# Kernel optimization log

Measured on AMD Instinct MI355X. Metric: run time of the kernel, lower is better.

The kernel has to match this reference:

```python
import jax, jax.numpy as jnp
import numpy as np

IOU_THRESHOLD = 0.5
ROIS_NUMBER = 256


def setup_inputs() -> dict:
    key = jax.random.key(0)
    k1, k2, k3 = jax.random.split(key, 3)
    B, N = 8, 4096
    scores = jax.random.uniform(k1, (B, N, 1), dtype=jnp.float32)
    xy = jax.random.uniform(k2, (B, N, 2), dtype=jnp.float32) * 100.0
    wh = jax.random.uniform(k3, (B, N, 2), dtype=jnp.float32) * 20.0 + 1.0
    return {"input": jnp.concatenate([scores, xy, wh], axis=-1)}


def _make_corners(regs):
    # regs: [N,4] = (x, y, w, h); TF uses floor-div by 2 (`//`) on floats
    x, y, w, h = regs[:, 0], regs[:, 1], regs[:, 2], regs[:, 3]
    ws = w // 2
    hs = h // 2
    return jnp.stack([x - ws, y - hs, x + ws, y + hs], axis=-1)


def _nms_single(preds, key):
    # preds: [N,5] = (score, x, y, w, h)
    N = preds.shape[0]
    scores = preds[:, 0]
    boxes = _make_corners(preds[:, 1:])
    order = jnp.argsort(-scores)                       # descending score
    b = boxes[order]
    x1, y1, x2, y2 = b[:, 0], b[:, 1], b[:, 2], b[:, 3]
    area = (x2 - x1) * (y2 - y1)
    # pairwise IoU [N,N] (selection only -> stop_gradient)
    ix1 = jnp.maximum(x1[:, None], x1[None, :])
    iy1 = jnp.maximum(y1[:, None], y1[None, :])
    ix2 = jnp.minimum(x2[:, None], x2[None, :])
    iy2 = jnp.minimum(y2[:, None], y2[None, :])
    inter = jnp.maximum(ix2 - ix1, 0.0) * jnp.maximum(iy2 - iy1, 0.0)
    union = area[:, None] + area[None, :] - inter
    iou = jax.lax.stop_gradient(jnp.where(union > 0, inter / union, 0.0))

    idx = jnp.arange(N)

    def step(suppressed, i):
        keep_i = ~suppressed[i]
        suppressed = suppressed | (keep_i & (iou[i] > IOU_THRESHOLD) & (idx > i))
        return suppressed, keep_i

    _, keep = jax.lax.scan(step, jnp.zeros((N,), bool), idx)

    # first ROIS_NUMBER kept positions (in score order); N marks "not kept"
    pos = jnp.sort(jnp.where(keep, idx, N))[:ROIS_NUMBER]
    valid = pos < N
    sel = order[jnp.minimum(pos, N - 1)]
    rand_idx = jax.random.randint(key, (ROIS_NUMBER,), 0, N)
    sel = jnp.where(valid, sel, rand_idx)              # pad with random regions
    return preds[sel][:, 1:]                           # [ROIS,4] = (x,y,w,h)


def reference(input) -> jnp.ndarray:
    B = input.shape[0]
    keys = jax.random.split(jax.random.key(42), B)
    return jax.vmap(_nms_single)(input, keys)
```

## Files before the change

### kernel.cpp

```cpp
#include <hip/hip_runtime.h>
#include <stdint.h>

#pragma clang fp contract(off)

#define NMS_B 8
#define NMS_N 4096
#define ROIS 256

typedef unsigned long long u64;
typedef unsigned int u32;

__device__ __forceinline__ int lds_slot(int e) { return e + (e >> 2); }

__device__ __forceinline__ bool sup_pred(float4 rc, float rh, float4 cc, float ch) {
    float iw = fmaxf(fminf(rc.z, cc.z) - fmaxf(rc.x, cc.x), 0.0f);
    float ih = fmaxf(fminf(rc.w, cc.w) - fmaxf(rc.y, cc.y), 0.0f);
    float inter = iw * ih;
    return inter > fmaf(-0.5f, inter, rh + ch);
}

__global__ __launch_bounds__(1024, 1) void nms_all(
        const float* __restrict__ in, u32* __restrict__ sortedIdx,
        float4* __restrict__ crn, float* __restrict__ ha,
        float* __restrict__ outp) {
    __shared__ u64 sm[5120];
    __shared__ int kept[ROIS];
    __shared__ int s_selCount, s_B, s_needFull;
    const int b = blockIdx.x, t = threadIdx.x;
    const int lane = t & 63, wid = t >> 6;
    const size_t base = (size_t)b * NMS_N;

    u32* hist = (u32*)sm;
    u32* pp   = (u32*)sm + 4096;
    u32* qq   = (u32*)sm + 5120;
    float sc[4];
    int   bk[4];
    #pragma unroll
    for (int r = 0; r < 4; ++r) {
        int e = t + 1024 * r;
        sc[r] = in[(base + e) * 5];
        int bb = (int)(sc[r] * 4096.0f);
        bk[r] = bb > 4095 ? 4095 : bb;
    }
    for (int i = t; i < 4096; i += 1024) hist[i] = 0;
    if (t == 0) { s_selCount = 0; s_needFull = 0; }
    __syncthreads();
    #pragma unroll
    for (int r = 0; r < 4; ++r) atomicAdd(&hist[bk[r]], 1u);
    __syncthreads();
    pp[t] = hist[4 * t] + hist[4 * t + 1] + hist[4 * t + 2] + hist[4 * t + 3];
    __syncthreads();
    if (t < 64) {
        u32 s = 0;
        for (int i = 0; i < 16; ++i) s += pp[16 * t + i];
        qq[t] = s;
    }
    __syncthreads();
    if (t == 0) {
        int acc = 0, L = 0;
        for (int l = 63; l >= 0; --l) { acc += (int)qq[l]; if (acc >= 512) { L = l; break; } }
        int rem = 512 - (acc - (int)qq[L]);
        int acc2 = 0, T = 16 * L;
        for (int i = 16 * L + 15; i >= 16 * L; --i) { acc2 += (int)pp[i]; if (acc2 >= rem) { T = i; break; } }
        int rem2 = rem - (acc2 - (int)pp[T]);
        int acc3 = 0, B = 4 * T;
        for (int bb = 4 * T + 3; bb >= 4 * T; --bb) { acc3 += (int)hist[bb]; if (acc3 >= rem2) { B = bb; break; } }
        s_B = B;
    }
    __syncthreads();

    u64* selKey = sm + 2560;
    const int B = s_B;
    #pragma unroll
    for (int r = 0; r < 4; ++r) {
        if (bk[r] >= B) {
            int slot = atomicAdd(&s_selCount, 1);
            if (slot < 1024) {
                int e = t + 1024 * r;
                selKey[slot] = ((u64)(~__float_as_uint(sc[r])) << 32) | (u32)e;
            }
        }
    }
    __syncthreads();
    const int selCount = s_selCount;
    const bool fullPath = (selCount > 1024);

    if (!fullPath) {
        u64 kk = (t < selCount) ? selKey[t] : ~0ULL;
        for (int k = 2; k <= 1024; k <<= 1) {
            int j = k >> 1;
            for (; j >= 64; j >>= 1) {
                sm[lds_slot(t)] = kk;
                __syncthreads();
                u64 part = sm[lds_slot(t ^ j)];
                bool up = ((t & k) == 0), lower = ((t & j) == 0);
                u64 mn = kk < part ? kk : part, mx = kk < part ? part : kk;
                kk = (up == lower) ? mn : mx;
                __syncthreads();
            }
            for (; j >= 1; j >>= 1) {
                u64 part = __shfl_xor(kk, j, 64);
                bool up = ((t & k) == 0), lower = ((t & j) == 0);
                u64 mn = kk < part ? kk : part, mx = kk < part ? part : kk;
                kk = (up == lower) ? mn : mx;
            }
        }
        selKey[t] = kk;
        __syncthreads();

        float4* crn_s = (float4*)((char*)sm + 28672);
        float*  ha_s  = (float*)((char*)sm + 36864);
        u32*    sidx_s = (u32*)((char*)sm + 38912);
        if (t < 512) {
            u32 orig = (u32)selKey[t];
            const float* bp = in + (base + orig) * 5;
            float x = bp[1], y = bp[2], w = bp[3], h = bp[4];
            float ws_ = floorf(w * 0.5f), hs_ = floorf(h * 0.5f);
            float4 c4 = make_float4(x - ws_, y - hs_, x + ws_, y + hs_);
            crn_s[t] = c4;
            ha_s[t] = 0.5f * ((c4.z - c4.x) * (c4.w - c4.y));
            sidx_s[t] = orig;
        }
        for (int r = t; r < ROIS; r += 1024) kept[r] = 0;
        __syncthreads();

        u64* h_lds = sm;
        for (int u = wid; u < 36; u += 16) {
            int kr = 0;
            while ((kr + 1) * (kr + 2) / 2 <= u) ++kr;
            int w = u - kr * (kr + 1) / 2;
            float4 myc = crn_s[64 * kr + lane];
            float  myh = ha_s[64 * kr + lane];
            u64 word = 0;
            #pragma unroll 4
            for (int q = 0; q < 64; ++q) {
                bool p = sup_pred(crn_s[64 * w + q], ha_s[64 * w + q], myc, myh);
                word |= ((u64)(p ? 1u : 0u)) << q;
            }
            h_lds[u * 64 + lane] = word;
        }
        __syncthreads();

        if (t < 64) {
            int count = 0;
            u32 f[8];
            #pragma unroll
            for (int k = 0; k < 8; ++k) f[k] = 1u;
            bool done = false;
            #pragma unroll
            for (int g = 0; g < 8; ++g) {
                if (!done) {
                    u64 hgg = h_lds[(g * (g + 1) / 2 + g) * 64 + lane];
                    u64 kb = 0;
                    u64 avail = __ballot(f[g] != 0);
                    while (avail != 0 && count < ROIS) {
                        int r = __builtin_ctzll(avail);
                        if (lane == 0) kept[count] = g * 64 + r;
                        ++count;
                        kb |= 1ULL << r;
                        u32 bit = (u32)(hgg >> r) & 1u;
                        f[g] &= (bit ^ 1u) & (u32)(lane != r);
                        avail = __ballot(f[g] != 0);
                    }
                    if (count >= ROIS) {
                        done = true;
                    } else {
                        #pragma unroll
                        for (int k2 = g + 1; k2 < 8; ++k2)
                            f[k2] &= (u32)((h_lds[(k2 * (k2 + 1) / 2 + g) * 64 + lane] & kb) == 0);
                    }
                }
            }
            if (t == 0) s_needFull = (count >= ROIS) ? 0 : 1;
        }
        __syncthreads();
    }

    if (fullPath || s_needFull) {
        u64 key[4];
        #pragma unroll
        for (int r = 0; r < 4; ++r) {
            int e = 4 * t + r;
            float s = in[(base + e) * 5];
            key[r] = ((u64)(~__float_as_uint(s)) << 32) | (u32)e;
        }
        for (int k = 2; k <= 4096; k <<= 1) {
            int j = k >> 1;
            if (j >= 256) {
                #pragma unroll
                for (int r = 0; r < 4; ++r) sm[lds_slot(4 * t + r)] = key[r];
                __syncthreads();
                for (; j >= 256; j >>= 1) {
                    for (int el = t; el < 4096; el += 1024) {
                        int p = el ^ j;
                        if (p > el) {
                            u64 a = sm[lds_slot(el)], cc = sm[lds_slot(p)];
                            bool up = ((el & k) == 0);
                            if ((a > cc) == up) { sm[lds_slot(el)] = cc; sm[lds_slot(p)] = a; }
                        }
                    }
                    __syncthreads();
                }
                #pragma unroll
                for (int r = 0; r < 4; ++r) key[r] = sm[lds_slot(4 * t + r)];
            }
            for (; j >= 4; j >>= 1) {
                int d = j >> 2;
                #pragma unroll
                for (int r = 0; r < 4; ++r) {
                    int e = 4 * t + r;
                    u64 mine = key[r];
                    u64 part = __shfl_xor(mine, d, 64);
                    bool up = ((e & k) == 0);
                    bool lower = ((e & j) == 0);
                    u64 mn = (mine < part) ? mine : part;
                    u64 mx = (mine < part) ? part : mine;
                    key[r] = (up == lower) ? mn : mx;
                }
            }
            for (; j >= 1; j >>= 1) {
                #pragma unroll
                for (int r = 0; r < 4; ++r) {
                    int pr = r | j;
                    if (((r & j) == 0) && pr < 4) {
                        int e = 4 * t + r;
                        bool up = ((e & k) == 0);
                        u64 a = key[r], cc = key[pr];
                        if ((a > cc) == up) { key[r] = cc; key[pr] = a; }
                    }
                }
            }
        }
        __syncthreads();

        u64*    h2 = sm;
        float4* crn2 = (float4*)(sm + 2304);
        float*  ha2  = (float*)(sm + 2304 + 1024);

        #pragma unroll
        for (int r = 0; r < 4; ++r) {
            int e = 4 * t + r;
            u32 orig = (u32)key[r];
            const float* bp = in + (base + orig) * 5;
            float x = bp[1], y = bp[2], w = bp[3], h = bp[4];
            float ws_ = floorf(w * 0.5f), hs_ = floorf(h * 0.5f);
            float4 c4 = make_float4(x - ws_, y - hs_, x + ws_, y + hs_);
            float hv = 0.5f * ((c4.z - c4.x) * (c4.w - c4.y));
            size_t g = base + e;
            sortedIdx[g] = orig;
            crn[g] = c4;
            ha[g] = hv;
            if (e < 512) { crn2[e] = c4; ha2[e] = hv; }
        }
        for (int r = t; r < ROIS; r += 1024) kept[r] = 0;
        __syncthreads();

        for (int u = wid; u < 36; u += 16) {
            int kr = 0;
            while ((kr + 1) * (kr + 2) / 2 <= u) ++kr;
            int w = u - kr * (kr + 1) / 2;
            float4 myc = crn2[64 * kr + lane];
            float  myh = ha2[64 * kr + lane];
            u64 word = 0;
            #pragma unroll 4
            for (int q = 0; q < 64; ++q) {
                bool p = sup_pred(crn2[64 * w + q], ha2[64 * w + q], myc, myh);
                word |= ((u64)(p ? 1u : 0u)) << q;
            }
            h2[(size_t)u * 64 + lane] = word;
        }
        __syncthreads();

        if (t < 64) {
            int count = 0;
            u32 f[8];
            #pragma unroll
            for (int k = 0; k < 8; ++k) f[k] = 1u;
            bool done = false;
            #pragma unroll
            for (int g = 0; g < 8; ++g) {
                if (!done) {
                    u64 hgg = h2[(size_t)(g * (g + 1) / 2 + g) * 64 + lane];
                    u64 kb = 0;
                    u64 avail = __ballot(f[g] != 0);
                    while (avail != 0 && count < ROIS) {
                        int r = __builtin_ctzll(avail);
                        if (lane == 0) kept[count] = g * 64 + r;
                        ++count;
                        kb |= 1ULL << r;
                        u32 bit = (u32)(hgg >> r) & 1u;
                        f[g] &= (bit ^ 1u) & (u32)(lane != r);
                        avail = __ballot(f[g] != 0);
                    }
                    if (count >= ROIS) {
                        done = true;
                    } else {
                        #pragma unroll
                        for (int k2 = g + 1; k2 < 8; ++k2)
                            f[k2] &= (u32)((h2[(size_t)(k2 * (k2 + 1) / 2 + g) * 64 + lane] & kb) == 0);
                    }
                }
            }
            if (count < ROIS) {
                for (int Wp = 4; Wp < 32 && count < ROIS; ++Wp) {
                    const int cLo = 128 * Wp + lane, cHi = cLo + 64;
                    float4 cL = crn[base + cLo]; float hL = ha[base + cLo];
                    float4 cH = crn[base + cHi]; float hH = ha[base + cHi];
                    u32 fLo = 1u, fHi = 1u;
                    for (int j2 = 0; j2 < count; ++j2) {
                        int pos = kept[j2];
                        float4 kc = crn[base + pos]; float kh = ha[base + pos];
                        fLo &= (u32)(!sup_pred(kc, kh, cL, hL));
                        fHi &= (u32)(!sup_pred(kc, kh, cH, hH));
                    }
                    u64 curLo0 = 0, curHi0 = 0, curHi1 = 0;
                    for (int r = 0; r < 64; ++r) {
                        float4 rc = crn[base + 128 * Wp + r]; float rh = ha[base + 128 * Wp + r];
                        curLo0 |= ((u64)(sup_pred(rc, rh, cL, hL) ? 1u : 0u)) << r;
                        curHi0 |= ((u64)(sup_pred(rc, rh, cH, hH) ? 1u : 0u)) << r;
                    }
                    for (int r = 0; r < 64; ++r) {
                        float4 rc = crn[base + 128 * Wp + 64 + r]; float rh = ha[base + 128 * Wp + 64 + r];
                        curHi1 |= ((u64)(sup_pred(rc, rh, cH, hH) ? 1u : 0u)) << r;
                    }
                    u64 availLo = __ballot(fLo != 0);
                    while (availLo != 0 && count < ROIS) {
                        int r = __builtin_ctzll(availLo);
                        if (lane == 0) kept[count] = Wp * 128 + r;
                        ++count;
                        fLo &= (u32)(((curLo0 >> r) & 1ULL) ^ 1ULL) & (u32)(lane != r);
                        fHi &= (u32)(((curHi0 >> r) & 1ULL) ^ 1ULL);
                        availLo = __ballot(fLo != 0);
                    }
                    u64 availHi = __ballot(fHi != 0);
                    while (availHi != 0 && count < ROIS) {
                        int r = __builtin_ctzll(availHi);
                        if (lane == 0) kept[count] = Wp * 128 + 64 + r;
                        ++count;
                        fHi &= (u32)(((curHi1 >> r) & 1ULL) ^ 1ULL) & (u32)(lane != r);
                        availHi = __ballot(fHi != 0);
                    }
                }
            }
        }
    }
    __syncthreads();

    const bool usedFull = fullPath || (s_needFull != 0);
    if (t < ROIS) {
        int pos = kept[t];
        int orig = usedFull ? (int)sortedIdx[base + pos]
                            : (int)((u32*)((char*)sm + 38912))[pos];
        const float* bp = in + (base + orig) * 5;
        ((float4*)outp)[(size_t)b * ROIS + t] =
            make_float4(bp[1], bp[2], bp[3], bp[4]);
    }
}

extern "C" void kernel_launch(void* const* d_in, const int* in_sizes, int n_in,
                              void* d_out, int out_size, void* d_ws, size_t ws_size,
                              hipStream_t stream) {
    const float* in = (const float*)d_in[0];
    float* out = (float*)d_out;
    char* ws = (char*)d_ws;

    u32* sortedIdx = (u32*)ws;                 size_t off = (size_t)NMS_B * NMS_N * 4;
    float4* crn = (float4*)(ws + off);         off += (size_t)NMS_B * NMS_N * 16;
    float* ha = (float*)(ws + off);            off += (size_t)NMS_B * NMS_N * 4;

    nms_all<<<NMS_B, 1024, 0, stream>>>(in, sortedIdx, crn, ha, out);
}
```

Baseline: 103.1 us.

## Sort four keys per thread, aggregate selection atomics, split IoU mask words

The 1024-element bitonic sort now runs on 256 threads holding four keys each. Only the strides of 256 and up go through LDS with barriers; smaller strides use wave shuffles and in-register compare-swaps, which removes most block-wide syncs. Candidate selection uses one ballot-based atomic per wave instead of one atomic per element. The IoU mask computation is split into 32-bit half-words so twice as many wave tasks share the work. Shared memory is re-laid out with dedicated regions, which raises LDS use, and a clamp of negative bucket indices is added.

```diff
diff --git a/kernel.cpp b/kernel.cpp
--- a/kernel.cpp
+++ b/kernel.cpp
@@ -23,16 +23,23 @@
         const float* __restrict__ in, u32* __restrict__ sortedIdx,
         float4* __restrict__ crn, float* __restrict__ ha,
         float* __restrict__ outp) {
-    __shared__ u64 sm[5120];
+    __shared__ u64 sm[8736];
     __shared__ int kept[ROIS];
     __shared__ int s_selCount, s_B, s_needFull;
     const int b = blockIdx.x, t = threadIdx.x;
     const int lane = t & 63, wid = t >> 6;
     const size_t base = (size_t)b * NMS_N;
 
-    u32* hist = (u32*)sm;
-    u32* pp   = (u32*)sm + 4096;
-    u32* qq   = (u32*)sm + 5120;
+    u32*    hist   = (u32*)sm;
+    u32*    pp     = (u32*)(sm + 2048);
+    u32*    qq     = (u32*)(sm + 2560);
+    u64*    selKey = sm + 2592;
+    u64*    sortA  = sm + 3616;
+    float4* crn_s  = (float4*)(sm + 4896);
+    float*  ha_s   = (float*)(sm + 5920);
+    u32*    sidx_s = (u32*)(sm + 6176);
+    u32*    h32    = (u32*)(sm + 6432);
+
     float sc[4];
     int   bk[4];
     #pragma unroll
@@ -40,6 +47,7 @@
         int e = t + 1024 * r;
         sc[r] = in[(base + e) * 5];
         int bb = (int)(sc[r] * 4096.0f);
+        bb = bb < 0 ? 0 : bb;
         bk[r] = bb > 4095 ? 4095 : bb;
     }
     for (int i = t; i < 4096; i += 1024) hist[i] = 0;
@@ -69,12 +77,17 @@
     }
     __syncthreads();
 
-    u64* selKey = sm + 2560;
     const int B = s_B;
     #pragma unroll
     for (int r = 0; r < 4; ++r) {
-        if (bk[r] >= B) {
-            int slot = atomicAdd(&s_selCount, 1);
+        bool pred = (bk[r] >= B);
+        u64 m = __ballot(pred);
+        u32 cnt = (u32)__popcll(m);
+        int wbase = 0;
+        if (lane == 0 && cnt) wbase = atomicAdd(&s_selCount, (int)cnt);
+        wbase = __shfl(wbase, 0, 64);
+        if (pred) {
+            int slot = wbase + (int)__popcll(m & ((1ULL << lane) - 1ULL));
             if (slot < 1024) {
                 int e = t + 1024 * r;
                 selKey[slot] = ((u64)(~__float_as_uint(sc[r])) << 32) | (u32)e;
@@ -86,31 +99,75 @@
     const bool fullPath = (selCount > 1024);
 
     if (!fullPath) {
-        u64 kk = (t < selCount) ? selKey[t] : ~0ULL;
+        u64 key4[4];
+        if (t < 256) {
+            #pragma unroll
+            for (int r = 0; r < 4; ++r) {
+                int e = 4 * t + r;
+                key4[r] = (e < selCount) ? selKey[e] : ~0ULL;
+            }
+        }
         for (int k = 2; k <= 1024; k <<= 1) {
             int j = k >> 1;
-            for (; j >= 64; j >>= 1) {
-                sm[lds_slot(t)] = kk;
+            if (j >= 256) {
+                if (t < 256) {
+                    #pragma unroll
+                    for (int r = 0; r < 4; ++r) sortA[lds_slot(4 * t + r)] = key4[r];
+                }
                 __syncthreads();
-                u64 part = sm[lds_slot(t ^ j)];
-                bool up = ((t & k) == 0), lower = ((t & j) == 0);
-                u64 mn = kk < part ? kk : part, mx = kk < part ? part : kk;
-                kk = (up == lower) ? mn : mx;
-                __syncthreads();
-            }
-            for (; j >= 1; j >>= 1) {
-                u64 part = __shfl_xor(kk, j, 64);
-                bool up = ((t & k) == 0), lower = ((t & j) == 0);
-                u64 mn = kk < part ? kk : part, mx = kk < part ? part : kk;
-                kk = (up == lower) ? mn : mx;
-            }
-        }
-        selKey[t] = kk;
-        __syncthreads();
-
-        float4* crn_s = (float4*)((char*)sm + 28672);
-        float*  ha_s  = (float*)((char*)sm + 36864);
-        u32*    sidx_s = (u32*)((char*)sm + 38912);
+                for (; j >= 256; j >>= 1) {
+                    if (t < 256) {
+                        for (int el = t; el < 1024; el += 256) {
+                            int p = el ^ j;
+                            if (p > el) {
+                                u64 a = sortA[lds_slot(el)], cc = sortA[lds_slot(p)];
+                                bool up = ((el & k) == 0);
+                                if ((a > cc) == up) { sortA[lds_slot(el)] = cc; sortA[lds_slot(p)] = a; }
+                            }
+                        }
+                    }
+                    __syncthreads();
+                }
+                if (t < 256) {
+                    #pragma unroll
+                    for (int r = 0; r < 4; ++r) key4[r] = sortA[lds_slot(4 * t + r)];
+                }
+            }
+            if (t < 256) {
+                for (; j >= 4; j >>= 1) {
+                    int d = j >> 2;
+                    #pragma unroll
+                    for (int r = 0; r < 4; ++r) {
+                        int e = 4 * t + r;
+                        u64 mine = key4[r];
+                        u64 part = __shfl_xor(mine, d, 64);
+                        bool up = ((e & k) == 0);
+                        bool lower = ((e & j) == 0);
+                        u64 mn = (mine < part) ? mine : part;
+                        u64 mx = (mine < part) ? part : mine;
+                        key4[r] = (up == lower) ? mn : mx;
+                    }
+                }
+                for (; j >= 1; j >>= 1) {
+                    #pragma unroll
+                    for (int r = 0; r < 4; ++r) {
+                        int pr = r | j;
+                        if (((r & j) == 0) && pr < 4) {
+                            int e = 4 * t + r;
+                            bool up = ((e & k) == 0);
+                            u64 a = key4[r], cc = key4[pr];
+                            if ((a > cc) == up) { key4[r] = cc; key4[pr] = a; }
+                        }
+                    }
+                }
+            }
+        }
+        if (t < 256) {
+            #pragma unroll
+            for (int r = 0; r < 4; ++r) selKey[4 * t + r] = key4[r];
+        }
+        __syncthreads();
+
         if (t < 512) {
             u32 orig = (u32)selKey[t];
             const float* bp = in + (base + orig) * 5;
@@ -124,24 +181,26 @@
         for (int r = t; r < ROIS; r += 1024) kept[r] = 0;
         __syncthreads();
 
-        u64* h_lds = sm;
-        for (int u = wid; u < 36; u += 16) {
+        for (int tau = wid; tau < 72; tau += 16) {
+            int u = tau >> 1, hf = tau & 1;
             int kr = 0;
             while ((kr + 1) * (kr + 2) / 2 <= u) ++kr;
             int w = u - kr * (kr + 1) / 2;
             float4 myc = crn_s[64 * kr + lane];
             float  myh = ha_s[64 * kr + lane];
-            u64 word = 0;
+            u32 word = 0;
+            const int q0 = hf * 32;
             #pragma unroll 4
-            for (int q = 0; q < 64; ++q) {
-                bool p = sup_pred(crn_s[64 * w + q], ha_s[64 * w + q], myc, myh);
-                word |= ((u64)(p ? 1u : 0u)) << q;
-            }
-            h_lds[u * 64 + lane] = word;
+            for (int q = 0; q < 32; ++q) {
+                bool p = sup_pred(crn_s[64 * w + q0 + q], ha_s[64 * w + q0 + q], myc, myh);
+                word |= (u32)(p ? 1u : 0u) << q;
+            }
+            h32[(u * 64 + lane) * 2 + hf] = word;
         }
         __syncthreads();
 
         if (t < 64) {
+            u64* h_lds = (u64*)h32;
             int count = 0;
             u32 f[8];
             #pragma unroll
@@ -350,7 +409,7 @@
     if (t < ROIS) {
         int pos = kept[t];
         int orig = usedFull ? (int)sortedIdx[base + pos]
-                            : (int)((u32*)((char*)sm + 38912))[pos];
+                            : (int)((u32*)(sm + 6176))[pos];
         const float* bp = in + (base + orig) * 5;
         ((float4*)outp)[(size_t)b * ROIS + t] =
             make_float4(bp[1], bp[2], bp[3], bp[4]);
```

After: 111.4 us. 8.1% more time.
